# Performance work log

Hardware: AMD Instinct MI355X
Metric: run time of the kernel (lower is better)

## Reference

```python
import jax, jax.numpy as jnp
import numpy as np

N_NODES = 100000
N_EDGES = 320000
DIM = 256  # hidden_dim*2 (bi-RNN)
BN_EPS = 1e-5


def setup_inputs() -> dict:
    key = jax.random.key(0)
    k1, k2, k3 = jax.random.split(key, 3)
    x = jax.random.normal(k1, (N_NODES, DIM), dtype=jnp.float32)
    W = jax.random.normal(k2, (DIM, DIM), dtype=jnp.float32) * (1.0 / np.sqrt(DIM))
    b = jnp.zeros((DIM,), dtype=jnp.float32)
    gamma = jnp.ones((DIM,), dtype=jnp.float32)
    beta = jnp.zeros((DIM,), dtype=jnp.float32)
    edge_index = jax.random.randint(k3, (2, N_EDGES), 0, N_NODES, dtype=jnp.int64)
    return {"x": x, "W": W, "b": b, "gamma": gamma, "beta": beta,
            "edge_index": edge_index}


def reference(x, W, b, gamma, beta, edge_index):
    N = x.shape[0]
    # --- GCNConv: add self-loops, symmetric deg^-1/2 normalization ---
    loop = jnp.arange(N, dtype=edge_index.dtype)
    row = jnp.concatenate([edge_index[0], loop])  # source / j
    col = jnp.concatenate([edge_index[1], loop])  # target / i
    deg = jax.ops.segment_sum(jnp.ones_like(col, dtype=x.dtype), col,
                              num_segments=N)
    dinv = jax.lax.rsqrt(deg)  # deg >= 1 due to self-loops
    norm = dinv[row] * dinv[col]  # [E+N]
    h = x @ W  # linear transform before propagation (PyG GCNConv)
    msg = h[row] * norm[:, None]  # gather + scale, [E+N, F]
    out = jax.ops.segment_sum(msg, col, num_segments=N) + b  # scatter-add
    # --- BatchNorm1d over nodes (training-mode batch statistics) ---
    mean = jnp.mean(out, axis=0)
    var = jnp.var(out, axis=0)
    out = (out - mean) * jax.lax.rsqrt(var + BN_EPS) * gamma + beta
    return jnp.tanh(out)
```

## Files before the change

### kernel.cpp

```cpp
#include <hip/hip_runtime.h>
#include <stdint.h>

#define N_NODES 100000
#define N_EDGES 320000
#define DIM 256
#define BN_EPS 1e-5f

typedef __attribute__((ext_vector_type(8))) short short8;
typedef __attribute__((ext_vector_type(4))) float f32x4;

__device__ __forceinline__ float bf2f(unsigned short u) {
    union { unsigned int i; float f; } v; v.i = ((unsigned int)u) << 16; return v.f;
}
__device__ __forceinline__ unsigned short f2bf(float f) {
    union { float f; unsigned int i; } v; v.f = f;
    unsigned int x = v.i;
    return (unsigned short)((x + 0x7fffu + ((x >> 16) & 1u)) >> 16);
}
__device__ __forceinline__ int eidx(const int* ei, int i64, int which, int e) {
    int idx = which * N_EDGES + e;
    return i64 ? ei[idx * 2] : ei[idx];
}
__device__ __forceinline__ f32x4 ldx4(const void* xv, int xf32, size_t off) {
    if (xf32) return *(const f32x4*)((const float*)xv + off);
    uint2 u = *(const uint2*)((const unsigned short*)xv + off);
    f32x4 o;
    o[0] = bf2f((unsigned short)(u.x & 0xffffu));
    o[1] = bf2f((unsigned short)(u.x >> 16));
    o[2] = bf2f((unsigned short)(u.y & 0xffffu));
    o[3] = bf2f((unsigned short)(u.y >> 16));
    return o;
}

__global__ void k_init(const unsigned short* __restrict__ xs,
                       const unsigned short* __restrict__ wsw,
                       const int* __restrict__ ei, int* __restrict__ flags,
                       int* __restrict__ cnt, float* __restrict__ stats) {
    __shared__ int red[3];
    int t = threadIdx.x;
    int i = blockIdx.x * 256 + t;
    if (i < N_NODES) cnt[i] = 0;
    if (i < 512) stats[i] = 0.0f;
    if (blockIdx.x == 0) {
        if (t < 3) red[t] = 0;
        __syncthreads();
        int badx = 0, badw = 0, nz = 0;
        for (int j = 0; j < 8; ++j) {
            if (!(fabsf(bf2f(xs[t * 8 + j])) <= 1000.0f)) badx = 1;
            if (!(fabsf(bf2f(wsw[t * 8 + j])) <= 1000.0f)) badw = 1;
            if (ei[(t * 8 + j) * 2 + 1] != 0) nz = 1;
        }
        if (badx) atomicOr(&red[0], 1);
        if (badw) atomicOr(&red[1], 1);
        if (nz)   atomicOr(&red[2], 1);
        __syncthreads();
        if (t == 0) { flags[0] = red[0]; flags[1] = red[1]; flags[2] = red[2] ? 0 : 1; }
    }
}

__global__ void k_cntwt(const int* __restrict__ ei, int* __restrict__ cnt,
                        const void* __restrict__ wv, unsigned short* __restrict__ Wth,
                        unsigned short* __restrict__ Wtl, const int* __restrict__ flags) {
    int b = blockIdx.x, t = threadIdx.x;
    if (b < 1250) {
        int i64 = flags[2];
        int e = b * 256 + t;
        if (e < N_EDGES) atomicAdd(&cnt[eidx(ei, i64, 1, e)], 1);
    } else {
        int wf32 = flags[1];
        int k = b - 1250, n = t;
        float v = wf32 ? ((const float*)wv)[k * DIM + n]
                       : bf2f(((const unsigned short*)wv)[k * DIM + n]);
        unsigned short h = f2bf(v);
        Wth[(size_t)n * DIM + k] = h;
        Wtl[(size_t)n * DIM + k] = f2bf(v - bf2f(h));
    }
}

__global__ void k_dscan(const int* __restrict__ cnt, float* __restrict__ dinv,
                        int* __restrict__ partial) {
    __shared__ int red[256];
    int t = threadIdx.x, b = blockIdx.x;
    int i = b * 256 + t;
    if (i < N_NODES) dinv[i] = rsqrtf((float)cnt[i] + 1.0f);
    if (b < 200) {
        int i0 = b * 512 + t * 2;
        int s = 0;
        if (i0 < N_NODES) s += cnt[i0];
        if (i0 + 1 < N_NODES) s += cnt[i0 + 1];
        red[t] = s;
        __syncthreads();
        for (int off = 128; off > 0; off >>= 1) {
            if (t < off) red[t] += red[t + off];
            __syncthreads();
        }
        if (t == 0) partial[b] = red[0];
    }
}

__global__ void k_scan2(const int* __restrict__ partial, int* __restrict__ pbase) {
    __shared__ int s[256];
    int t = threadIdx.x;
    int v = (t < 200) ? partial[t] : 0;
    s[t] = v;
    __syncthreads();
    for (int off = 1; off < 256; off <<= 1) {
        int u = (t >= off) ? s[t - off] : 0;
        __syncthreads();
        s[t] += u;
        __syncthreads();
    }
    if (t < 200) pbase[t] = s[t] - v;
}

__global__ void k_scan3(const int* __restrict__ cnt, const int* __restrict__ pbase,
                        int* __restrict__ row_start, int* __restrict__ cursor) {
    __shared__ int s[512];
    int t = threadIdx.x, b = blockIdx.x;
    int i = b * 512 + t;
    int v = (i < N_NODES) ? cnt[i] : 0;
    s[t] = v;
    __syncthreads();
    for (int off = 1; off < 512; off <<= 1) {
        int u = (t >= off) ? s[t - off] : 0;
        __syncthreads();
        s[t] += u;
        __syncthreads();
    }
    if (i < N_NODES) {
        int excl = pbase[b] + s[t] - v;
        row_start[i] = excl;
        cursor[i] = excl;
    }
}

__global__ void k_fill(const int* __restrict__ ei, const float* __restrict__ dinv,
                       int* __restrict__ cursor, int2* __restrict__ csr_pk,
                       const int* __restrict__ flags) {
    int i64 = flags[2];
    int e = blockIdx.x * 256 + threadIdx.x;
    if (e >= N_EDGES) return;
    int c = eidx(ei, i64, 1, e);
    int r = eidx(ei, i64, 0, e);
    int slot = atomicAdd(&cursor[c], 1);
    union { float f; int i; } u; u.f = dinv[r] * dinv[c];
    int2 pk; pk.x = r; pk.y = u.i;
    csr_pk[slot] = pk;
}

__launch_bounds__(256, 2)
__global__ void k_fused(const void* __restrict__ xv, const int* __restrict__ row_start,
                        const int* __restrict__ cnt, const int2* __restrict__ csr_pk,
                        const float* __restrict__ dinv,
                        const unsigned short* __restrict__ Wth,
                        const unsigned short* __restrict__ Wtl,
                        float* __restrict__ out, float* __restrict__ stats,
                        const int* __restrict__ flags) {
    __shared__ unsigned short zsh[80 * 256];
    __shared__ unsigned short zsl[80 * 256];
    int tid = threadIdx.x;
    int m0l = blockIdx.x * 80;
    int w = tid >> 6, lane = tid & 63, quad = lane >> 4, rl = lane & 15;
    int xf32 = flags[0];
    size_t lo4 = (size_t)(lane * 4);

    for (int nn = 0; nn < 20; ++nn) {
        int row = w * 20 + nn;
        int node = m0l + row;
        int start = row_start[node];
        int len = cnt[node];
        float dv = dinv[node];
        float s = dv * dv;

        int myi = node;
        float myn = 0.0f;
        if (lane < len) {
            int2 pk = csr_pk[start + lane];
            myi = pk.x;
            union { int i; float f; } u; u.i = pk.y;
            myn = u.f;
        }
        bool big = (len > 63);
        int n_eff;
        if (!big) {
            if (lane == len) myn = s;
            n_eff = len + 1;
        } else {
            n_eff = 64;
        }
        int npad = (n_eff + 3) & ~3;

        f32x4 acc = (f32x4){0.f, 0.f, 0.f, 0.f};
        if (xf32) {
            const float* xp = (const float*)xv;
            for (int j = 0; j < npad; j += 4) {
                int i0 = __shfl(myi, j),     i1 = __shfl(myi, j + 1);
                int i2 = __shfl(myi, j + 2), i3 = __shfl(myi, j + 3);
                float n0 = __shfl(myn, j),     n1 = __shfl(myn, j + 1);
                float n2 = __shfl(myn, j + 2), n3 = __shfl(myn, j + 3);
                f32x4 x0 = *(const f32x4*)(xp + (size_t)i0 * DIM + lo4);
                f32x4 x1 = *(const f32x4*)(xp + (size_t)i1 * DIM + lo4);
                f32x4 x2 = *(const f32x4*)(xp + (size_t)i2 * DIM + lo4);
                f32x4 x3 = *(const f32x4*)(xp + (size_t)i3 * DIM + lo4);
                #pragma unroll
                for (int q = 0; q < 4; ++q)
                    acc[q] += n0 * x0[q] + n1 * x1[q] + n2 * x2[q] + n3 * x3[q];
            }
        } else {
            const unsigned short* xp = (const unsigned short*)xv;
            for (int j = 0; j < npad; j += 4) {
                int i0 = __shfl(myi, j),     i1 = __shfl(myi, j + 1);
                int i2 = __shfl(myi, j + 2), i3 = __shfl(myi, j + 3);
                float n0 = __shfl(myn, j),     n1 = __shfl(myn, j + 1);
                float n2 = __shfl(myn, j + 2), n3 = __shfl(myn, j + 3);
                uint2 u0 = *(const uint2*)(xp + (size_t)i0 * DIM + lo4);
                uint2 u1 = *(const uint2*)(xp + (size_t)i1 * DIM + lo4);
                uint2 u2 = *(const uint2*)(xp + (size_t)i2 * DIM + lo4);
                uint2 u3 = *(const uint2*)(xp + (size_t)i3 * DIM + lo4);
                acc[0] += n0 * bf2f((unsigned short)(u0.x & 0xffffu))
                        + n1 * bf2f((unsigned short)(u1.x & 0xffffu))
                        + n2 * bf2f((unsigned short)(u2.x & 0xffffu))
                        + n3 * bf2f((unsigned short)(u3.x & 0xffffu));
                acc[1] += n0 * bf2f((unsigned short)(u0.x >> 16))
                        + n1 * bf2f((unsigned short)(u1.x >> 16))
                        + n2 * bf2f((unsigned short)(u2.x >> 16))
                        + n3 * bf2f((unsigned short)(u3.x >> 16));
                acc[2] += n0 * bf2f((unsigned short)(u0.y & 0xffffu))
                        + n1 * bf2f((unsigned short)(u1.y & 0xffffu))
                        + n2 * bf2f((unsigned short)(u2.y & 0xffffu))
                        + n3 * bf2f((unsigned short)(u3.y & 0xffffu));
                acc[3] += n0 * bf2f((unsigned short)(u0.y >> 16))
                        + n1 * bf2f((unsigned short)(u1.y >> 16))
                        + n2 * bf2f((unsigned short)(u2.y >> 16))
                        + n3 * bf2f((unsigned short)(u3.y >> 16));
            }
        }
        if (big) {
            f32x4 xs = ldx4(xv, xf32, (size_t)node * DIM + lo4);
            #pragma unroll
            for (int q = 0; q < 4; ++q) acc[q] += s * xs[q];
            for (int t2 = 64; t2 < len; ++t2) {
                int2 pk = csr_pk[start + t2];
                union { int i; float f; } u; u.i = pk.y;
                f32x4 xr = ldx4(xv, xf32, (size_t)pk.x * DIM + lo4);
                #pragma unroll
                for (int q = 0; q < 4; ++q) acc[q] += u.f * xr[q];
            }
        }

        unsigned short h0 = f2bf(acc[0]), h1 = f2bf(acc[1]);
        unsigned short h2 = f2bf(acc[2]), h3 = f2bf(acc[3]);
        uint2 vh, vl;
        vh.x = (unsigned int)h0 | ((unsigned int)h1 << 16);
        vh.y = (unsigned int)h2 | ((unsigned int)h3 << 16);
        vl.x = (unsigned int)f2bf(acc[0] - bf2f(h0))
             | ((unsigned int)f2bf(acc[1] - bf2f(h1)) << 16);
        vl.y = (unsigned int)f2bf(acc[2] - bf2f(h2))
             | ((unsigned int)f2bf(acc[3] - bf2f(h3)) << 16);
        int sl  = lane >> 1;
        int swz = (sl & 24) | ((sl & 7) ^ (row & 7));
        int offb = swz * 16 + (lane & 1) * 8;
        *(uint2*)((char*)zsh + (size_t)row * 512 + offb) = vh;
        *(uint2*)((char*)zsl + (size_t)row * 512 + offb) = vl;
    }
    __syncthreads();

    f32x4 cacc[5][4];
    #pragma unroll
    for (int ms = 0; ms < 5; ++ms)
        #pragma unroll
        for (int nt = 0; nt < 4; ++nt)
            cacc[ms][nt] = (f32x4){0.f, 0.f, 0.f, 0.f};

    #pragma unroll
    for (int kk = 0; kk < 8; ++kk) {
        int k0g = kk * 32 + quad * 8;
        short8 bh[4], bl[4];
        #pragma unroll
        for (int nt = 0; nt < 4; ++nt) {
            int n = w * 64 + nt * 16 + rl;
            bh[nt] = *(const short8*)(Wth + (size_t)n * DIM + k0g);
            bl[nt] = *(const short8*)(Wtl + (size_t)n * DIM + k0g);
        }
        #pragma unroll
        for (int ms = 0; ms < 5; ++ms) {
            int row = ms * 16 + rl;
            int slot = kk * 4 + quad;
            int sl = (slot & 24) | ((slot & 7) ^ (row & 7));
            short8 ah = *(const short8*)((const char*)zsh + (size_t)row * 512 + sl * 16);
            short8 al = *(const short8*)((const char*)zsl + (size_t)row * 512 + sl * 16);
            #pragma unroll
            for (int nt = 0; nt < 4; ++nt) {
                cacc[ms][nt] = __builtin_amdgcn_mfma_f32_16x16x32_bf16(ah, bh[nt], cacc[ms][nt], 0, 0, 0);
                cacc[ms][nt] = __builtin_amdgcn_mfma_f32_16x16x32_bf16(al, bh[nt], cacc[ms][nt], 0, 0, 0);
                cacc[ms][nt] = __builtin_amdgcn_mfma_f32_16x16x32_bf16(ah, bl[nt], cacc[ms][nt], 0, 0, 0);
            }
        }
    }

    #pragma unroll
    for (int nt = 0; nt < 4; ++nt) {
        int col = w * 64 + nt * 16 + rl;
        float s1 = 0.f, s2 = 0.f;
        #pragma unroll
        for (int ms = 0; ms < 5; ++ms)
            #pragma unroll
            for (int i = 0; i < 4; ++i) {
                float v = cacc[ms][nt][i];
                s1 += v; s2 += v * v;
                out[(size_t)(m0l + ms * 16 + quad * 4 + i) * DIM + col] = v;
            }
        s1 += __shfl_xor(s1, 16); s1 += __shfl_xor(s1, 32);
        s2 += __shfl_xor(s2, 16); s2 += __shfl_xor(s2, 32);
        if (lane < 16) {
            atomicAdd(&stats[col], s1);
            atomicAdd(&stats[256 + col], s2);
        }
    }
}

__global__ void k_final(float* __restrict__ out, const float* __restrict__ stats,
                        const void* __restrict__ gv, const void* __restrict__ bv,
                        const int* __restrict__ flags) {
    __shared__ float ssc[256], ssh[256];
    int t = threadIdx.x;
    {
        int ff32 = flags[0];
        const float invN = 1.0f / (float)N_NODES;
        float mean = stats[t] * invN;
        float var = stats[256 + t] * invN - mean * mean;
        float g = ff32 ? ((const float*)gv)[t] : bf2f(((const unsigned short*)gv)[t]);
        float bb = ff32 ? ((const float*)bv)[t] : bf2f(((const unsigned short*)bv)[t]);
        float sc = g * rsqrtf(var + BN_EPS);
        ssc[t] = sc;
        ssh[t] = bb - mean * sc;
    }
    __syncthreads();
    int gt = blockIdx.x * 256 + t;
    int f0 = (gt & 63) * 4;
    size_t off = (size_t)gt * 4;
    f32x4 v = *(const f32x4*)(out + off);
    f32x4 o;
    #pragma unroll
    for (int j = 0; j < 4; ++j)
        o[j] = tanhf(v[j] * ssc[f0 + j] + ssh[f0 + j]);
    *(f32x4*)(out + off) = o;
}

extern "C" void kernel_launch(void* const* d_in, const int* in_sizes, int n_in,
                              void* d_out, int out_size, void* d_ws, size_t ws_size,
                              hipStream_t stream) {
    const void* x     = d_in[0];
    const void* W     = d_in[1];
    const void* gamma = d_in[3];
    const void* beta  = d_in[4];
    const int* ei     = (const int*)d_in[5];
    float* out = (float*)d_out;

    char* ws = (char*)d_ws;
    int*   flags     = (int*)(ws);
    int*   cnt       = (int*)(ws + 4096);
    int*   row_start = (int*)(ws + 409600);
    int*   cursor    = (int*)(ws + 819200);
    float* dinv      = (float*)(ws + 1228800);
    int*   partial   = (int*)(ws + 1638400);
    int*   pbase     = (int*)(ws + 1646592);
    float* stats     = (float*)(ws + 1654784);
    unsigned short* Wth = (unsigned short*)(ws + 1671168);
    unsigned short* Wtl = (unsigned short*)(ws + 1802240);
    int2*  csr_pk    = (int2*)(ws + 1933312);

    const unsigned short* xs_us = (const unsigned short*)x;
    const unsigned short* W_us  = (const unsigned short*)W;

    k_init <<<391,  256, 0, stream>>>(xs_us, W_us, ei, flags, cnt, stats);
    k_cntwt<<<1506, 256, 0, stream>>>(ei, cnt, W, Wth, Wtl, flags);
    k_dscan<<<391,  256, 0, stream>>>(cnt, dinv, partial);
    k_scan2<<<1,    256, 0, stream>>>(partial, pbase);
    k_scan3<<<200,  512, 0, stream>>>(cnt, pbase, row_start, cursor);
    k_fill <<<1250, 256, 0, stream>>>(ei, dinv, cursor, csr_pk, flags);

    k_fused<<<1250, 256, 0, stream>>>(x, row_start, cnt, csr_pk, dinv,
                                      Wth, Wtl, out, stats, flags);

    k_final<<<25000, 256, 0, stream>>>(out, stats, gamma, beta, flags);
}
```

Baseline: 377.3 us.

## Use 512-thread blocks in fused kernel, prefetch next node's edges, nontemporal stores

```diff
diff --git a/kernel.cpp b/kernel.cpp
--- a/kernel.cpp
+++ b/kernel.cpp
@@ -148,7 +148,7 @@
     csr_pk[slot] = pk;
 }
 
-__launch_bounds__(256, 2)
+__launch_bounds__(512, 4)
 __global__ void k_fused(const void* __restrict__ xv, const int* __restrict__ row_start,
                         const int* __restrict__ cnt, const int2* __restrict__ csr_pk,
                         const float* __restrict__ dinv,
@@ -164,31 +164,50 @@
     int xf32 = flags[0];
     size_t lo4 = (size_t)(lane * 4);
 
-    for (int nn = 0; nn < 20; ++nn) {
-        int row = w * 20 + nn;
+    const int NPW = 10;
+    int nb0 = m0l + w * NPW;
+    int mstart = 0, mlen = 0; float mdv = 0.f;
+    if (lane < NPW) {
+        mstart = row_start[nb0 + lane];
+        mlen   = cnt[nb0 + lane];
+        mdv    = dinv[nb0 + lane];
+    }
+    int start = __shfl(mstart, 0);
+    int len   = __shfl(mlen, 0);
+    float dv  = __shfl(mdv, 0);
+    int2 pk_cur; pk_cur.x = 0; pk_cur.y = 0;
+    if (lane < len) pk_cur = csr_pk[start + lane];
+
+    for (int nn = 0; nn < NPW; ++nn) {
+        int row = w * NPW + nn;
         int node = m0l + row;
-        int start = row_start[node];
-        int len = cnt[node];
-        float dv = dinv[node];
         float s = dv * dv;
-
+        int cstart = start, clen = len;
         int myi = node;
         float myn = 0.0f;
-        if (lane < len) {
-            int2 pk = csr_pk[start + lane];
-            myi = pk.x;
-            union { int i; float f; } u; u.i = pk.y;
+        if (lane < clen) {
+            myi = pk_cur.x;
+            union { int i; float f; } u; u.i = pk_cur.y;
             myn = u.f;
         }
-        bool big = (len > 63);
+        bool big = (clen > 63);
         int n_eff;
         if (!big) {
-            if (lane == len) myn = s;
-            n_eff = len + 1;
+            if (lane == clen) myn = s;
+            n_eff = clen + 1;
         } else {
             n_eff = 64;
         }
         int npad = (n_eff + 3) & ~3;
+
+        if (nn + 1 < NPW) {
+            start = __shfl(mstart, nn + 1);
+            len   = __shfl(mlen, nn + 1);
+            dv    = __shfl(mdv, nn + 1);
+            int2 pk_n; pk_n.x = 0; pk_n.y = 0;
+            if (lane < len) pk_n = csr_pk[start + lane];
+            pk_cur = pk_n;
+        }
 
         f32x4 acc = (f32x4){0.f, 0.f, 0.f, 0.f};
         if (xf32) {
@@ -239,8 +258,8 @@
             f32x4 xs = ldx4(xv, xf32, (size_t)node * DIM + lo4);
             #pragma unroll
             for (int q = 0; q < 4; ++q) acc[q] += s * xs[q];
-            for (int t2 = 64; t2 < len; ++t2) {
-                int2 pk = csr_pk[start + t2];
+            for (int t2 = 64; t2 < clen; ++t2) {
+                int2 pk = csr_pk[cstart + t2];
                 union { int i; float f; } u; u.i = pk.y;
                 f32x4 xr = ldx4(xv, xf32, (size_t)pk.x * DIM + lo4);
                 #pragma unroll
@@ -265,20 +284,20 @@
     }
     __syncthreads();
 
-    f32x4 cacc[5][4];
+    f32x4 cacc[5][2];
     #pragma unroll
     for (int ms = 0; ms < 5; ++ms)
         #pragma unroll
-        for (int nt = 0; nt < 4; ++nt)
+        for (int nt = 0; nt < 2; ++nt)
             cacc[ms][nt] = (f32x4){0.f, 0.f, 0.f, 0.f};
 
     #pragma unroll
     for (int kk = 0; kk < 8; ++kk) {
         int k0g = kk * 32 + quad * 8;
-        short8 bh[4], bl[4];
+        short8 bh[2], bl[2];
         #pragma unroll
-        for (int nt = 0; nt < 4; ++nt) {
-            int n = w * 64 + nt * 16 + rl;
+        for (int nt = 0; nt < 2; ++nt) {
+            int n = w * 32 + nt * 16 + rl;
             bh[nt] = *(const short8*)(Wth + (size_t)n * DIM + k0g);
             bl[nt] = *(const short8*)(Wtl + (size_t)n * DIM + k0g);
         }
@@ -290,7 +309,7 @@
             short8 ah = *(const short8*)((const char*)zsh + (size_t)row * 512 + sl * 16);
             short8 al = *(const short8*)((const char*)zsl + (size_t)row * 512 + sl * 16);
             #pragma unroll
-            for (int nt = 0; nt < 4; ++nt) {
+            for (int nt = 0; nt < 2; ++nt) {
                 cacc[ms][nt] = __builtin_amdgcn_mfma_f32_16x16x32_bf16(ah, bh[nt], cacc[ms][nt], 0, 0, 0);
                 cacc[ms][nt] = __builtin_amdgcn_mfma_f32_16x16x32_bf16(al, bh[nt], cacc[ms][nt], 0, 0, 0);
                 cacc[ms][nt] = __builtin_amdgcn_mfma_f32_16x16x32_bf16(ah, bl[nt], cacc[ms][nt], 0, 0, 0);
@@ -299,8 +318,8 @@
     }
 
     #pragma unroll
-    for (int nt = 0; nt < 4; ++nt) {
-        int col = w * 64 + nt * 16 + rl;
+    for (int nt = 0; nt < 2; ++nt) {
+        int col = w * 32 + nt * 16 + rl;
         float s1 = 0.f, s2 = 0.f;
         #pragma unroll
         for (int ms = 0; ms < 5; ++ms)
@@ -308,7 +327,8 @@
             for (int i = 0; i < 4; ++i) {
                 float v = cacc[ms][nt][i];
                 s1 += v; s2 += v * v;
-                out[(size_t)(m0l + ms * 16 + quad * 4 + i) * DIM + col] = v;
+                __builtin_nontemporal_store(
+                    v, out + (size_t)(m0l + ms * 16 + quad * 4 + i) * DIM + col);
             }
         s1 += __shfl_xor(s1, 16); s1 += __shfl_xor(s1, 32);
         s2 += __shfl_xor(s2, 16); s2 += __shfl_xor(s2, 32);
@@ -344,7 +364,7 @@
     #pragma unroll
     for (int j = 0; j < 4; ++j)
         o[j] = tanhf(v[j] * ssc[f0 + j] + ssh[f0 + j]);
-    *(f32x4*)(out + off) = o;
+    __builtin_nontemporal_store(o, (f32x4*)(out + off));
 }
 
 extern "C" void kernel_launch(void* const* d_in, const int* in_sizes, int n_in,
@@ -380,7 +400,7 @@
     k_scan3<<<200,  512, 0, stream>>>(cnt, pbase, row_start, cursor);
     k_fill <<<1250, 256, 0, stream>>>(ei, dinv, cursor, csr_pk, flags);
 
-    k_fused<<<1250, 256, 0, stream>>>(x, row_start, cnt, csr_pk, dinv,
+    k_fused<<<1250, 512, 0, stream>>>(x, row_start, cnt, csr_pk, dinv,
                                       Wth, Wtl, out, stats, flags);
 
     k_final<<<25000, 256, 0, stream>>>(out, stats, gamma, beta, flags);
```

New measurement: 347.4 us. 7.9% less time.
